# Optimization experiments

Measured on AMD Instinct MI355X. Metric: run time of the kernel, lower is better.

## Reference

```python
import jax, jax.numpy as jnp
import numpy as np

HID = 1024
N_HEADS = 16
HEAD_DIM = HID // N_HEADS  # 64
SCALE = float(np.sqrt(HEAD_DIM))  # 8.0
# dba_l1 constants from the source
SCALING = float(np.sqrt(0.72676)) * SCALE
CENTER = SCALE ** 2 * 1.12838


def setup_inputs() -> dict:
    key = jax.random.key(0)
    kq, kk, kv = jax.random.split(key, 3)
    B, LQ, LK = 4, 256, 2048
    return {
        "attention_q": jax.random.normal(kq, (B, LQ, HID), dtype=jnp.float32),
        "attention_k": jax.random.normal(kk, (B, LK, HID), dtype=jnp.float32),
        "attention_v": jax.random.normal(kv, (B, LK, HID), dtype=jnp.float32),
        "attn_diag": jnp.ones((N_HEADS, 1, HEAD_DIM), dtype=jnp.float32),
    }


def _dba_l1_logits(Q, K, attn_diag):
    # Q: [B,H,Lq,D], K: [B,H,Lk,D], attn_diag: [H,1,D]
    # Scan over query positions (mirrors the original per-query loop) to avoid
    # materializing the [B,H,Lq,Lk,D] diff tensor.
    qs = jnp.moveaxis(Q, 2, 0)  # [Lq,B,H,D]

    def step(carry, qi):
        # qi: [B,H,D] -> dist: [B,H,Lk]
        dist = jnp.sum(attn_diag * jnp.abs(K - qi[:, :, None, :]), axis=-1)
        # (dist - CENTER) / (-SCALING) == (CENTER - dist) / SCALING
        return carry, (CENTER - dist) / SCALING

    _, logits = jax.lax.scan(step, None, qs)  # [Lq,B,H,Lk]
    return jnp.moveaxis(logits, 0, 2)  # [B,H,Lq,Lk]


def reference(attention_q, attention_k, attention_v, attn_diag):
    B, Lq, _ = attention_q.shape
    Lk = attention_k.shape[1]
    # split heads: [B,L,hid] -> [B,H,L,D]
    Q = attention_q.reshape(B, Lq, N_HEADS, HEAD_DIM).transpose(0, 2, 1, 3)
    K = attention_k.reshape(B, Lk, N_HEADS, HEAD_DIM).transpose(0, 2, 1, 3)
    V = attention_v.reshape(B, Lk, N_HEADS, HEAD_DIM).transpose(0, 2, 1, 3)

    attn_logits = _dba_l1_logits(Q, K, attn_diag)  # [B,H,Lq,Lk]
    attention = jax.nn.softmax(attn_logits, axis=-1)
    x = jnp.einsum("bhqk,bhkd->bhqd", attention, V)  # [B,H,Lq,D]
    output = x.transpose(0, 2, 1, 3).reshape(B, Lq, HID)
    return output, attention
```

## Files before the change

### kernel.cpp

```cpp
#include <hip/hip_runtime.h>
#include <stdint.h>

typedef _Float16 half_t;
typedef _Float16 h8_t __attribute__((ext_vector_type(8)));
typedef float f4 __attribute__((ext_vector_type(4)));
typedef unsigned int u4v __attribute__((ext_vector_type(4)));

#define NB 4
#define NH 16
#define HD 64
#define LQ 256
#define LK 2048
#define HIDN 1024

#define KF 0.21153832f
#define QS 2048.0f
#define PSTR 2056

__device__ __forceinline__ uint32_t sad16(uint32_t a, uint32_t b, uint32_t c) {
#if __has_builtin(__builtin_amdgcn_sad_u16)
  return __builtin_amdgcn_sad_u16(a, b, c);
#else
  int a0 = a & 0xffff, a1 = a >> 16, b0 = b & 0xffff, b1 = b >> 16;
  int d0 = a0 - b0, d1 = a1 - b1;
  return c + (uint32_t)(d0 < 0 ? -d0 : d0) + (uint32_t)(d1 < 0 ? -d1 : d1);
#endif
}
__device__ __forceinline__ uint32_t umin32(uint32_t a, uint32_t b) { return a < b ? a : b; }

__device__ __forceinline__ uint32_t quant2(float x0, float x1, float w0, float w1) {
  float f0 = fmaf(x0, w0, 32768.5f);
  float f1 = fmaf(x1, w1, 32768.5f);
  uint32_t u0 = (uint32_t)fminf(fmaxf(f0, 0.f), 65535.f);
  uint32_t u1 = (uint32_t)fminf(fmaxf(f1, 0.f), 65535.f);
  return u0 | (u1 << 16);
}

__global__ __launch_bounds__(256) void k_prep4(const float* __restrict__ Kin,
                                               const float* __restrict__ Vin,
                                               const float* __restrict__ diag,
                                               uint32_t* __restrict__ Ktq,
                                               half_t* __restrict__ Vfrag) {
  int bid = blockIdx.x;
  int isV = bid >= NB * NH * 32;
  int id = isV ? bid - NB * NH * 32 : bid;
  int kb = id & 31, bh = id >> 5, b = bh >> 4, h = bh & 15;
  int t = threadIdx.x;
  __shared__ float ls[64][65];
  {
    const float* base = isV ? Vin : Kin;
    int d = t & 63, kr = t >> 6;
    const float* src = base + (size_t)(b * LK + kb * 64 + kr) * HIDN + h * HD + d;
#pragma unroll
    for (int i = 0; i < 16; ++i) ls[kr + 4 * i][d] = src[(size_t)(4 * i) * HIDN];
  }
  __syncthreads();
  if (!isV) {
    int k = t & 63, g = t >> 6;
    uint32_t* dst = Ktq + ((size_t)bh * 32 + g * 8) * LK + kb * 64 + k;
#pragma unroll
    for (int i = 0; i < 8; ++i) {
      int d2 = g * 8 + i;
      float w0 = diag[h * HD + 2 * d2] * QS;
      float w1 = diag[h * HD + 2 * d2 + 1] * QS;
      dst[(size_t)i * LK] = quant2(ls[k][2 * d2], ls[k][2 * d2 + 1], w0, w1);
    }
  } else {
    half_t* dst = Vfrag + (size_t)bh * (HD * LK) + (size_t)kb * 4096;
#pragma unroll
    for (int i = 0; i < 2; ++i) {
      int s = t * 2 + i;
      int kcl = s >> 8, nt = (s >> 6) & 3, ln = s & 63;
      int kr = kcl * 32 + (ln >> 4) * 8;
      int n = nt * 16 + (ln & 15);
      h8_t v;
#pragma unroll
      for (int j = 0; j < 8; ++j) v[j] = (half_t)ls[kr + j][n];
      *(h8_t*)(dst + (size_t)s * 8) = v;
    }
  }
}

__global__ __launch_bounds__(256, 4) void k_fused(const float* __restrict__ Qin,
                                                  const uint32_t* __restrict__ Ktq,
                                                  const float* __restrict__ diag,
                                                  const half_t* __restrict__ Vfrag,
                                                  float* __restrict__ attn,
                                                  float* __restrict__ Xout) {
  int bid = blockIdx.x;
  int bh = bid & 63, qt = bid >> 6;
  int b = bh >> 4, h = bh & 15;
  int q0 = qt * 8, t = threadIdx.x;
  int lane = t & 63, wid = t >> 6;
  int m = lane & 15, quad = lane >> 4;

  __shared__ uint32_t Qsp[8][32];
  __shared__ float redf[4][8];
  __shared__ uint32_t redu[4][8];
  __shared__ __align__(16) char ShBuf[8 * PSTR * 2];
  half_t* Pst = (half_t*)ShBuf;
  float* Cred = (float*)ShBuf;

  {
    int q = t >> 5, d2 = t & 31;
    const float* qr = Qin + (size_t)(b * LQ + q0 + q) * HIDN + h * HD;
    float2 f = ((const float2*)qr)[d2];
    float2 w = ((const float2*)(diag + h * HD))[d2];
    Qsp[q][d2] = quant2(f.x, f.y, w.x * QS, w.y * QS);
  }
  __syncthreads();

  uint32_t acc[8][8];
#pragma unroll
  for (int q = 0; q < 8; ++q)
#pragma unroll
    for (int k = 0; k < 8; ++k) acc[q][k] = 0u;

  const uint32_t* kp = Ktq + (size_t)bh * 32 * LK + t * 8;
#pragma unroll 2
  for (int g = 0; g < 16; ++g) {
    u4v ka0 = *(const u4v*)kp;
    u4v ka1 = *(const u4v*)(kp + 4);
    u4v kb0 = *(const u4v*)(kp + LK);
    u4v kb1 = *(const u4v*)(kp + LK + 4);
    kp += 2 * LK;
#pragma unroll
    for (int q = 0; q < 8; ++q) {
      uint2 qd = *(const uint2*)&Qsp[q][2 * g];
#pragma unroll
      for (int k = 0; k < 4; ++k) {
        acc[q][k] = sad16(kb0[k], qd.y, sad16(ka0[k], qd.x, acc[q][k]));
        acc[q][4 + k] = sad16(kb1[k], qd.y, sad16(ka1[k], qd.x, acc[q][4 + k]));
      }
    }
  }

  uint32_t mrow[8];
#pragma unroll
  for (int q = 0; q < 8; ++q) {
    uint32_t mn = acc[q][0];
#pragma unroll
    for (int k = 1; k < 8; ++k) mn = umin32(mn, acc[q][k]);
#pragma unroll
    for (int off = 32; off; off >>= 1)
      mn = umin32(mn, (uint32_t)__shfl_xor((int)mn, off, 64));
    mrow[q] = mn;
  }
  if (lane == 0) {
#pragma unroll
    for (int q = 0; q < 8; ++q) redu[wid][q] = mrow[q];
  }
  __syncthreads();
#pragma unroll
  for (int q = 0; q < 8; ++q)
    mrow[q] = umin32(umin32(redu[0][q], redu[1][q]), umin32(redu[2][q], redu[3][q]));
  __syncthreads();

  const float KFQ = KF / QS;
  float pv[8][8];
  float rsum[8];
#pragma unroll
  for (int q = 0; q < 8; ++q) {
    float s = 0.f;
#pragma unroll
    for (int k = 0; k < 8; ++k) {
      float p = exp2f((float)((int)mrow[q] - (int)acc[q][k]) * KFQ);
      pv[q][k] = p;
      s += p;
    }
#pragma unroll
    for (int off = 32; off; off >>= 1) s += __shfl_xor(s, off, 64);
    rsum[q] = s;
  }
  if (lane == 0) {
#pragma unroll
    for (int q = 0; q < 8; ++q) redf[wid][q] = rsum[q];
  }
  __syncthreads();
#pragma unroll
  for (int q = 0; q < 8; ++q)
    rsum[q] = (redf[0][q] + redf[1][q]) + (redf[2][q] + redf[3][q]);

#pragma unroll
  for (int q = 0; q < 8; ++q) {
    float inv = 1.0f / rsum[q];
    f4 p0, p1;
    h8_t hp;
#pragma unroll
    for (int i = 0; i < 4; ++i) {
      p0[i] = pv[q][i] * inv;
      p1[i] = pv[q][4 + i] * inv;
      hp[i] = (half_t)p0[i];
      hp[4 + i] = (half_t)p1[i];
    }
    size_t row = (size_t)(bh * LQ + q0 + q) * LK + t * 8;
    ((f4*)(attn + row))[0] = p0;
    ((f4*)(attn + row))[1] = p1;
    *(h8_t*)(Pst + q * PSTR + t * 8) = hp;
  }

  f4 cfr[4];
#pragma unroll
  for (int nt = 0; nt < 4; ++nt) cfr[nt] = (f4){0.f, 0.f, 0.f, 0.f};
  const half_t* vf = Vfrag + (size_t)bh * (HD * LK);
#pragma unroll 2
  for (int c = 0; c < 16; ++c) {
    int kc = wid * 16 + c;
    h8_t af = *(const h8_t*)(Pst + (m & 7) * PSTR + kc * 32 + quad * 8);
#pragma unroll
    for (int nt = 0; nt < 4; ++nt) {
      h8_t bf = *(const h8_t*)(vf + (size_t)((kc * 4 + nt) * 64 + lane) * 8);
      cfr[nt] = __builtin_amdgcn_mfma_f32_16x16x32_f16(af, bf, cfr[nt], 0, 0, 0);
    }
  }

  __syncthreads();
  if (quad < 2) {
#pragma unroll
    for (int nt = 0; nt < 4; ++nt)
#pragma unroll
      for (int r = 0; r < 4; ++r)
        Cred[((wid * 8 + quad * 4 + r) * 64) + nt * 16 + m] = cfr[nt][r];
  }
  __syncthreads();

  {
    int q = t >> 5, d0 = (t & 31) * 2;
    float s0 = 0.f, s1 = 0.f;
#pragma unroll
    for (int w = 0; w < 4; ++w) {
      s0 += Cred[((w * 8 + q) * 64) + d0];
      s1 += Cred[((w * 8 + q) * 64) + d0 + 1];
    }
    float2 o = {s0, s1};
    *(float2*)(Xout + (size_t)(b * LQ + q0 + q) * HIDN + h * HD + d0) = o;
  }
}

__global__ __launch_bounds__(256, 2) void k_attn_slow(const float* __restrict__ Qin,
                                                      const float* __restrict__ Kin,
                                                      const float* __restrict__ diag,
                                                      float* __restrict__ attn) {
  int bid = blockIdx.x;
  int qt = bid & 15, bh = bid >> 4;
  int b = bh >> 4, h = bh & 15;
  int q0 = qt * 16, t = threadIdx.x;
  __shared__ float Qs[16][64];
  __shared__ float Dg[64];
  __shared__ float red[4][16];
  {
    int q = t >> 4;
    const f4* src = (const f4*)(Qin + (size_t)(b * LQ + q0 + q) * HIDN + h * HD);
    ((f4*)Qs[q])[t & 15] = src[t & 15];
  }
  if (t < 64) Dg[t] = diag[h * HD + t];
  __syncthreads();
  float acc[16][8];
#pragma unroll
  for (int q = 0; q < 16; ++q)
#pragma unroll
    for (int j = 0; j < 8; ++j) acc[q][j] = 0.f;
  const float* kfp = Kin + (size_t)(b * LK + t * 8) * HIDN + h * HD;
  for (int d = 0; d < 64; ++d) {
    float dgd = Dg[d];
    float kd[8];
#pragma unroll
    for (int j = 0; j < 8; ++j) kd[j] = kfp[(size_t)j * HIDN + d];
#pragma unroll
    for (int j = 0; j < 8; ++j) {
      float kv = kd[j];
#pragma unroll
      for (int q = 0; q < 16; ++q)
        acc[q][j] = fmaf(dgd, fabsf(kv - Qs[q][d]), acc[q][j]);
    }
  }
  int lane = t & 63, wid = t >> 6;
  float mrow[16];
#pragma unroll
  for (int q = 0; q < 16; ++q) {
    float mm = acc[q][0];
#pragma unroll
    for (int j = 1; j < 8; ++j) mm = fminf(mm, acc[q][j]);
#pragma unroll
    for (int off = 32; off; off >>= 1) mm = fminf(mm, __shfl_xor(mm, off, 64));
    mrow[q] = mm;
  }
  if (lane == 0)
#pragma unroll
    for (int q = 0; q < 16; ++q) red[wid][q] = mrow[q];
  __syncthreads();
#pragma unroll
  for (int q = 0; q < 16; ++q)
    mrow[q] = fminf(fminf(red[0][q], red[1][q]), fminf(red[2][q], red[3][q]));
  __syncthreads();
  float rsum[16];
#pragma unroll
  for (int q = 0; q < 16; ++q) {
    float s = 0.f;
#pragma unroll
    for (int j = 0; j < 8; ++j) {
      float p = exp2f((mrow[q] - acc[q][j]) * KF);
      acc[q][j] = p;
      s += p;
    }
#pragma unroll
    for (int off = 32; off; off >>= 1) s += __shfl_xor(s, off, 64);
    rsum[q] = s;
  }
  if (lane == 0)
#pragma unroll
    for (int q = 0; q < 16; ++q) red[wid][q] = rsum[q];
  __syncthreads();
#pragma unroll
  for (int q = 0; q < 16; ++q)
    rsum[q] = (red[0][q] + red[1][q]) + (red[2][q] + red[3][q]);
#pragma unroll
  for (int q = 0; q < 16; ++q) {
    float inv = 1.0f / rsum[q];
    f4 p0, p1;
#pragma unroll
    for (int i = 0; i < 4; ++i) { p0[i] = acc[q][i] * inv; p1[i] = acc[q][4 + i] * inv; }
    float* op = attn + ((size_t)(bh * LQ + q0 + q)) * LK + t * 8;
    ((f4*)op)[0] = p0;
    ((f4*)op)[1] = p1;
  }
}

__global__ __launch_bounds__(256) void k_pv_old(const float* __restrict__ P,
                                                const float* __restrict__ Vin,
                                                float* __restrict__ Xout) {
  int bid = blockIdx.x;
  int qt = bid & 3, bh = bid >> 2;
  int b = bh >> 4, h = bh & 15;
  int q0 = qt * 64;
  int t = threadIdx.x, lane = t & 63, wid = t >> 6;
  int m = lane & 15, quad = lane >> 4;
  __shared__ half_t Vts[64 * 256];
  f4 cfr[4];
#pragma unroll
  for (int nt = 0; nt < 4; ++nt) cfr[nt] = (f4){0.f, 0.f, 0.f, 0.f};
  int qrow = q0 + wid * 16 + m;
  const float* pbase = P + ((size_t)(bh * LQ + qrow)) * LK + quad * 8;
  for (int kb = 0; kb < 8; ++kb) {
    {
      int d = wid * 16 + (lane & 15);
      int kg = lane >> 4;
      const float* vp = Vin + (size_t)(b * LK + kb * 256) * HIDN + h * HD + d;
#pragma unroll
      for (int i = 0; i < 32; ++i) {
        int kl = i * 8 + kg * 2;
        float v0 = vp[(size_t)kl * HIDN];
        float v1 = vp[(size_t)(kl + 1) * HIDN];
        int addr = d * 256 + ((((kl >> 3) ^ (d & 7)) << 3) | (kl & 7));
        Vts[addr] = (half_t)v0;
        Vts[addr + 1] = (half_t)v1;
      }
    }
    __syncthreads();
#pragma unroll
    for (int ks = 0; ks < 8; ++ks) {
      const float* pp = pbase + kb * 256 + ks * 32;
      f4 a0 = ((const f4*)pp)[0];
      f4 a1 = ((const f4*)pp)[1];
      h8_t af;
#pragma unroll
      for (int i = 0; i < 4; ++i) { af[i] = (half_t)a0[i]; af[4 + i] = (half_t)a1[i]; }
      int koff = ks * 32 + quad * 8;
#pragma unroll
      for (int nt = 0; nt < 4; ++nt) {
        int n = nt * 16 + m;
        int vaddr = n * 256 + ((((koff >> 3) ^ (n & 7)) << 3));
        h8_t bf = *(const h8_t*)&Vts[vaddr];
        cfr[nt] = __builtin_amdgcn_mfma_f32_16x16x32_f16(af, bf, cfr[nt], 0, 0, 0);
      }
    }
    __syncthreads();
  }
#pragma unroll
  for (int nt = 0; nt < 4; ++nt)
#pragma unroll
    for (int r = 0; r < 4; ++r) {
      int row = quad * 4 + r;
      int q = q0 + wid * 16 + row;
      Xout[(size_t)(b * LQ + q) * HIDN + h * HD + nt * 16 + m] = cfr[nt][r];
    }
}

extern "C" void kernel_launch(void* const* d_in, const int* in_sizes, int n_in,
                              void* d_out, int out_size, void* d_ws, size_t ws_size,
                              hipStream_t stream) {
  const float* Q = (const float*)d_in[0];
  const float* K = (const float*)d_in[1];
  const float* V = (const float*)d_in[2];
  const float* dg = (const float*)d_in[3];
  float* out = (float*)d_out;
  float* attn = out + (size_t)NB * LQ * HIDN;

  size_t ktB = (size_t)NB * NH * 32 * LK * 4;
  size_t vfB = (size_t)NB * NH * HD * LK * 2;
  char* wsb = (char*)d_ws;
  uint32_t* Ktq = (uint32_t*)wsb;
  half_t* Vfrag = (half_t*)(wsb + ktB);

  if (ws_size >= ktB + vfB) {
    k_prep4<<<NB * NH * 32 * 2, 256, 0, stream>>>(K, V, dg, Ktq, Vfrag);
    k_fused<<<NB * NH * 32, 256, 0, stream>>>(Q, Ktq, dg, Vfrag, attn, out);
  } else {
    k_attn_slow<<<NB * NH * 16, 256, 0, stream>>>(Q, K, dg, attn);
    k_pv_old<<<NB * NH * 4, 256, 0, stream>>>(attn, V, out);
  }
}
```

Measured before the change: 268.9 us.

## Split fused attention block across 512 threads with 4 keys per thread

Doubles the threads per block in the fused L1-distance attention kernel, so each thread handles 4 keys instead of 8 and each wave covers half as many PV chunks. Cross-wave reductions move to an 8-wave transposed layout read with vector loads, and one redundant barrier is dropped. Attention and output stores become nontemporal. The aim is more parallelism and fewer registers per thread, at the cost of more shuffle-reduction overhead per key and a larger final cross-wave sum.

```diff
diff --git a/kernel.cpp b/kernel.cpp
--- a/kernel.cpp
+++ b/kernel.cpp
@@ -3,6 +3,7 @@
 
 typedef _Float16 half_t;
 typedef _Float16 h8_t __attribute__((ext_vector_type(8)));
+typedef _Float16 h4_t __attribute__((ext_vector_type(4)));
 typedef float f4 __attribute__((ext_vector_type(4)));
 typedef unsigned int u4v __attribute__((ext_vector_type(4)));
 
@@ -81,7 +82,7 @@
   }
 }
 
-__global__ __launch_bounds__(256, 4) void k_fused(const float* __restrict__ Qin,
+__global__ __launch_bounds__(512, 8) void k_fused(const float* __restrict__ Qin,
                                                   const uint32_t* __restrict__ Ktq,
                                                   const float* __restrict__ diag,
                                                   const half_t* __restrict__ Vfrag,
@@ -95,13 +96,13 @@
   int m = lane & 15, quad = lane >> 4;
 
   __shared__ uint32_t Qsp[8][32];
-  __shared__ float redf[4][8];
-  __shared__ uint32_t redu[4][8];
+  __shared__ float redf[8][8];
+  __shared__ uint32_t redu[8][8];
   __shared__ __align__(16) char ShBuf[8 * PSTR * 2];
   half_t* Pst = (half_t*)ShBuf;
   float* Cred = (float*)ShBuf;
 
-  {
+  if (t < 256) {
     int q = t >> 5, d2 = t & 31;
     const float* qr = Qin + (size_t)(b * LQ + q0 + q) * HIDN + h * HD;
     float2 f = ((const float2*)qr)[d2];
@@ -110,37 +111,31 @@
   }
   __syncthreads();
 
-  uint32_t acc[8][8];
+  uint32_t acc[8][4];
 #pragma unroll
   for (int q = 0; q < 8; ++q)
 #pragma unroll
-    for (int k = 0; k < 8; ++k) acc[q][k] = 0u;
-
-  const uint32_t* kp = Ktq + (size_t)bh * 32 * LK + t * 8;
+    for (int k = 0; k < 4; ++k) acc[q][k] = 0u;
+
+  const uint32_t* kp = Ktq + (size_t)bh * 32 * LK + t * 4;
 #pragma unroll 2
   for (int g = 0; g < 16; ++g) {
-    u4v ka0 = *(const u4v*)kp;
-    u4v ka1 = *(const u4v*)(kp + 4);
-    u4v kb0 = *(const u4v*)(kp + LK);
-    u4v kb1 = *(const u4v*)(kp + LK + 4);
+    u4v ka = *(const u4v*)kp;
+    u4v kb = *(const u4v*)(kp + LK);
     kp += 2 * LK;
 #pragma unroll
     for (int q = 0; q < 8; ++q) {
       uint2 qd = *(const uint2*)&Qsp[q][2 * g];
 #pragma unroll
-      for (int k = 0; k < 4; ++k) {
-        acc[q][k] = sad16(kb0[k], qd.y, sad16(ka0[k], qd.x, acc[q][k]));
-        acc[q][4 + k] = sad16(kb1[k], qd.y, sad16(ka1[k], qd.x, acc[q][4 + k]));
-      }
+      for (int k = 0; k < 4; ++k)
+        acc[q][k] = sad16(kb[k], qd.y, sad16(ka[k], qd.x, acc[q][k]));
     }
   }
 
   uint32_t mrow[8];
 #pragma unroll
   for (int q = 0; q < 8; ++q) {
-    uint32_t mn = acc[q][0];
-#pragma unroll
-    for (int k = 1; k < 8; ++k) mn = umin32(mn, acc[q][k]);
+    uint32_t mn = umin32(umin32(acc[q][0], acc[q][1]), umin32(acc[q][2], acc[q][3]));
 #pragma unroll
     for (int off = 32; off; off >>= 1)
       mn = umin32(mn, (uint32_t)__shfl_xor((int)mn, off, 64));
@@ -148,22 +143,25 @@
   }
   if (lane == 0) {
 #pragma unroll
-    for (int q = 0; q < 8; ++q) redu[wid][q] = mrow[q];
-  }
-  __syncthreads();
-#pragma unroll
-  for (int q = 0; q < 8; ++q)
-    mrow[q] = umin32(umin32(redu[0][q], redu[1][q]), umin32(redu[2][q], redu[3][q]));
-  __syncthreads();
+    for (int q = 0; q < 8; ++q) redu[q][wid] = mrow[q];
+  }
+  __syncthreads();
+#pragma unroll
+  for (int q = 0; q < 8; ++q) {
+    u4v a = *(const u4v*)&redu[q][0];
+    u4v c = *(const u4v*)&redu[q][4];
+    mrow[q] = umin32(umin32(umin32(a[0], a[1]), umin32(a[2], a[3])),
+                     umin32(umin32(c[0], c[1]), umin32(c[2], c[3])));
+  }
 
   const float KFQ = KF / QS;
-  float pv[8][8];
+  float pv[8][4];
   float rsum[8];
 #pragma unroll
   for (int q = 0; q < 8; ++q) {
     float s = 0.f;
 #pragma unroll
-    for (int k = 0; k < 8; ++k) {
+    for (int k = 0; k < 4; ++k) {
       float p = exp2f((float)((int)mrow[q] - (int)acc[q][k]) * KFQ);
       pv[q][k] = p;
       s += p;
@@ -174,29 +172,29 @@
   }
   if (lane == 0) {
 #pragma unroll
-    for (int q = 0; q < 8; ++q) redf[wid][q] = rsum[q];
-  }
-  __syncthreads();
-#pragma unroll
-  for (int q = 0; q < 8; ++q)
-    rsum[q] = (redf[0][q] + redf[1][q]) + (redf[2][q] + redf[3][q]);
+    for (int q = 0; q < 8; ++q) redf[q][wid] = rsum[q];
+  }
+  __syncthreads();
+#pragma unroll
+  for (int q = 0; q < 8; ++q) {
+    f4 a = *(const f4*)&redf[q][0];
+    f4 c = *(const f4*)&redf[q][4];
+    rsum[q] = ((a[0] + a[1]) + (a[2] + a[3])) + ((c[0] + c[1]) + (c[2] + c[3]));
+  }
 
 #pragma unroll
   for (int q = 0; q < 8; ++q) {
     float inv = 1.0f / rsum[q];
-    f4 p0, p1;
-    h8_t hp;
+    f4 p;
+    h4_t hp;
 #pragma unroll
     for (int i = 0; i < 4; ++i) {
-      p0[i] = pv[q][i] * inv;
-      p1[i] = pv[q][4 + i] * inv;
-      hp[i] = (half_t)p0[i];
-      hp[4 + i] = (half_t)p1[i];
-    }
-    size_t row = (size_t)(bh * LQ + q0 + q) * LK + t * 8;
-    ((f4*)(attn + row))[0] = p0;
-    ((f4*)(attn + row))[1] = p1;
-    *(h8_t*)(Pst + q * PSTR + t * 8) = hp;
+      p[i] = pv[q][i] * inv;
+      hp[i] = (half_t)p[i];
+    }
+    size_t row = (size_t)(bh * LQ + q0 + q) * LK + t * 4;
+    __builtin_nontemporal_store(p, (f4*)(attn + row));
+    *(h4_t*)(Pst + q * PSTR + t * 4) = hp;
   }
 
   f4 cfr[4];
@@ -204,8 +202,8 @@
   for (int nt = 0; nt < 4; ++nt) cfr[nt] = (f4){0.f, 0.f, 0.f, 0.f};
   const half_t* vf = Vfrag + (size_t)bh * (HD * LK);
 #pragma unroll 2
-  for (int c = 0; c < 16; ++c) {
-    int kc = wid * 16 + c;
+  for (int c = 0; c < 8; ++c) {
+    int kc = wid * 8 + c;
     h8_t af = *(const h8_t*)(Pst + (m & 7) * PSTR + kc * 32 + quad * 8);
 #pragma unroll
     for (int nt = 0; nt < 4; ++nt) {
@@ -225,15 +223,11 @@
   __syncthreads();
 
   {
-    int q = t >> 5, d0 = (t & 31) * 2;
-    float s0 = 0.f, s1 = 0.f;
-#pragma unroll
-    for (int w = 0; w < 4; ++w) {
-      s0 += Cred[((w * 8 + q) * 64) + d0];
-      s1 += Cred[((w * 8 + q) * 64) + d0 + 1];
-    }
-    float2 o = {s0, s1};
-    *(float2*)(Xout + (size_t)(b * LQ + q0 + q) * HIDN + h * HD + d0) = o;
+    int q = t >> 6, d = t & 63;
+    float s = 0.f;
+#pragma unroll
+    for (int w = 0; w < 8; ++w) s += Cred[((w * 8 + q) * 64) + d];
+    __builtin_nontemporal_store(s, Xout + (size_t)(b * LQ + q0 + q) * HIDN + h * HD + d);
   }
 }
 
@@ -404,7 +398,7 @@
 
   if (ws_size >= ktB + vfB) {
     k_prep4<<<NB * NH * 32 * 2, 256, 0, stream>>>(K, V, dg, Ktq, Vfrag);
-    k_fused<<<NB * NH * 32, 256, 0, stream>>>(Q, Ktq, dg, Vfrag, attn, out);
+    k_fused<<<NB * NH * 32, 512, 0, stream>>>(Q, Ktq, dg, Vfrag, attn, out);
   } else {
     k_attn_slow<<<NB * NH * 16, 256, 0, stream>>>(Q, K, dg, attn);
     k_pv_old<<<NB * NH * 4, 256, 0, stream>>>(attn, V, out);
```

After: 263.0 us. 2.2% less time.
